# Kernel tuning notes

Measured on AMD Instinct MI355X. Metric: run time of the kernel, lower is better.

Reference implementation:

```python
import jax, jax.numpy as jnp
import numpy as np

N, E, H, L, IN, OUT = 50000, 800000, 64, 14, 128, 112
MSG_EPS = 1e-7   # GENConv message epsilon
LN_EPS = 1e-5    # torch.nn.LayerNorm default eps


def setup_inputs() -> dict:
    key = jax.random.key(0)
    ks = jax.random.split(key, 8)
    s = 0.05
    x = jax.random.normal(ks[0], (N, IN), jnp.float32)
    edge_index = jax.random.randint(ks[1], (2, E), 0, N, dtype=jnp.int64)
    enc_W = jax.random.normal(ks[2], (IN, H), jnp.float32) * s
    enc_b = jnp.zeros((H,), jnp.float32)
    ln_g = jnp.ones((L, H), jnp.float32)
    ln_b = jnp.zeros((L, H), jnp.float32)
    mlp_W = jax.random.normal(ks[3], (L, H, H), jnp.float32) * s
    mlp_b = jnp.zeros((L, H), jnp.float32)
    pred_W = jax.random.normal(ks[4], (H, OUT), jnp.float32) * s
    pred_b = jnp.zeros((OUT,), jnp.float32)
    return dict(x=x, edge_index=edge_index, enc_W=enc_W, enc_b=enc_b,
                ln_g=ln_g, ln_b=ln_b, mlp_W=mlp_W, mlp_b=mlp_b,
                pred_W=pred_W, pred_b=pred_b)


def _layernorm(h, g, b):
    mu = jnp.mean(h, axis=-1, keepdims=True)
    var = jnp.mean(jnp.square(h - mu), axis=-1, keepdims=True)  # biased, as torch
    return (h - mu) * jax.lax.rsqrt(var + LN_EPS) * g + b


def _genconv(h, src, dst, W, b):
    # GENConv: msg = relu(x_src) + eps; softmax aggregation (t=1) over dst; out = Linear(x + agg)
    msg = jax.nn.relu(h[src]) + MSG_EPS                    # [E, H]
    mmax = jax.ops.segment_max(msg, dst, num_segments=N)   # [N, H]
    mmax = jnp.where(jnp.isfinite(mmax), mmax, 0.0)         # empty segments
    ex = jnp.exp(msg - mmax[dst])                           # [E, H]
    denom = jax.ops.segment_sum(ex, dst, num_segments=N)    # [N, H]
    num = jax.ops.segment_sum(msg * ex, dst, num_segments=N)
    agg = num / jnp.maximum(denom, 1e-16)                   # 0 for isolated nodes
    return (h + agg) @ W + b


def reference(x, edge_index, enc_W, enc_b, ln_g, ln_b, mlp_W, mlp_b, pred_W, pred_b):
    src, dst = edge_index[0], edge_index[1]
    h = x @ enc_W + enc_b                       # node feature encoder
    h = _genconv(h, src, dst, mlp_W[0], mlp_b[0])  # first GCN (no pre-norm in res+)

    def body(h, params):
        g, bl, W, b = params
        h2 = jax.nn.relu(_layernorm(h, g, bl))  # dropout is identity (eval)
        h = _genconv(h2, src, dst, W, b) + h    # residual
        return h, None

    h, _ = jax.lax.scan(body, h, (ln_g[:L - 1], ln_b[:L - 1], mlp_W[1:], mlp_b[1:]))
    return h @ pred_W + pred_b
```

## Files before the change

kernel.cpp:

```cpp
#include <hip/hip_runtime.h>
#include <hip/hip_bf16.h>

#define NN 50000
#define EE 800000
#define HD 64
#define LL 14
#define IND 128
#define OUTD 112
#define LN2 0.69314718056f

typedef __attribute__((ext_vector_type(8))) short short8;
typedef __attribute__((ext_vector_type(4))) float float4_;
typedef __attribute__((ext_vector_type(4))) unsigned short ushort4_;

__device__ __forceinline__ short bf16_hi(float x) {
    return (short)(__float_as_uint(x) >> 16);
}
__device__ __forceinline__ float bf16_f(short s) {
    return __uint_as_float(((unsigned)(unsigned short)s) << 16);
}
__device__ __forceinline__ float us2f(unsigned short u) {
    return __uint_as_float(((unsigned)u) << 16);
}
__device__ __forceinline__ unsigned short f2b_rne(float x) {
    unsigned u = __float_as_uint(x);
    u += 0x7fffu + ((u >> 16) & 1u);
    return (unsigned short)(u >> 16);
}

__device__ __forceinline__ void split8(const float* p, short8& hi, short8& lo) {
    float4_ a = *(const float4_*)p;
    float4_ b = *(const float4_*)(p + 4);
    float v[8] = {a[0], a[1], a[2], a[3], b[0], b[1], b[2], b[3]};
    #pragma unroll
    for (int j = 0; j < 8; ++j) {
        short h = bf16_hi(v[j]);
        hi[j] = h;
        lo[j] = bf16_hi(v[j] - bf16_f(h));
    }
}

__device__ __forceinline__ void load_b(const float* __restrict__ W, int ldw,
                                       int colbase, int krow, short8& hi, short8& lo) {
    #pragma unroll
    for (int j = 0; j < 8; ++j) {
        float wv = W[(krow + j) * ldw + colbase];
        short h = bf16_hi(wv);
        hi[j] = h;
        lo[j] = bf16_hi(wv - bf16_f(h));
    }
}

__device__ __forceinline__ float4_ mm3(short8 ah, short8 al, short8 bh, short8 bl,
                                       float4_ acc) {
    acc = __builtin_amdgcn_mfma_f32_16x16x32_bf16(ah, bh, acc, 0, 0, 0);
    acc = __builtin_amdgcn_mfma_f32_16x16x32_bf16(al, bh, acc, 0, 0, 0);
    acc = __builtin_amdgcn_mfma_f32_16x16x32_bf16(ah, bl, acc, 0, 0, 0);
    return acc;
}


__global__ void k_hist(const int* __restrict__ ei, int* __restrict__ cnt,
                       int* __restrict__ rank) {
    int e = blockIdx.x * blockDim.x + threadIdx.x;
    if (e < EE) rank[e] = atomicAdd(&cnt[ei[EE + e]], 1);
}

__global__ __launch_bounds__(1024) void k_scan1(const int* __restrict__ deg,
                                                int* __restrict__ excl,
                                                int* __restrict__ bsum) {
    __shared__ int ws[16];
    int tid = threadIdx.x, lane = tid & 63, w = tid >> 6;
    int gid = blockIdx.x * 1024 + tid;
    int v = (gid < NN) ? deg[gid] : 0;
    int x = v;
    #pragma unroll
    for (int d = 1; d < 64; d <<= 1) {
        int y = __shfl_up(x, d);
        if (lane >= d) x += y;
    }
    if (lane == 63) ws[w] = x;
    __syncthreads();
    if (tid == 0) {
        int acc = 0;
        for (int i = 0; i < 16; i++) { int t = ws[i]; ws[i] = acc; acc += t; }
        bsum[blockIdx.x] = acc;
    }
    __syncthreads();
    if (gid < NN) excl[gid] = x - v + ws[w];
}

__global__ void k_scan2(const int* __restrict__ bsum, int* __restrict__ boff, int nb) {
    if (threadIdx.x == 0) {
        int acc = 0;
        for (int i = 0; i < nb; i++) { boff[i] = acc; acc += bsum[i]; }
    }
}

__global__ __launch_bounds__(1024) void k_scan3(int* __restrict__ rp,
                                                const int* __restrict__ boff) {
    int gid = blockIdx.x * 1024 + threadIdx.x;
    if (gid < NN) rp[gid] += boff[blockIdx.x];
    if (gid == 0) rp[NN] = EE;
}

__global__ void k_scatter(const int* __restrict__ ei, const int* __restrict__ rp,
                          const int* __restrict__ rank, int* __restrict__ csrc) {
    int e = blockIdx.x * blockDim.x + threadIdx.x;
    if (e < EE) {
        int d = ei[EE + e];
        csrc[rp[d] + rank[e]] = ei[e];
    }
}


__global__ __launch_bounds__(256) void k_enc(const float* __restrict__ x,
                                             const float* __restrict__ W,
                                             const float* __restrict__ b,
                                             float* __restrict__ h,
                                             unsigned short* __restrict__ P0) {
    __shared__ float X[16 * 132];
    int tid = threadIdx.x, lane = tid & 63, w = tid >> 6;
    int nb = blockIdx.x * 16;
    int nq = lane >> 4, nr = lane & 15;
    int colbase = w * 16 + nr;

    {
        const float* src = x + (size_t)nb * IND + tid * 8;
        float4_ a = *(const float4_*)src;
        float4_ c = *(const float4_*)(src + 4);
        int m = tid >> 4, k8 = 8 * (tid & 15);
        *(float4_*)&X[m * 132 + k8] = a;
        *(float4_*)&X[m * 132 + k8 + 4] = c;
    }
    __syncthreads();

    float4_ acc = {};
    #pragma unroll
    for (int t = 0; t < 4; ++t) {
        short8 ah, al, bh, bl;
        split8(&X[nr * 132 + t * 32 + nq * 8], ah, al);
        load_b(W, HD, colbase, t * 32 + nq * 8, bh, bl);
        acc = mm3(ah, al, bh, bl, acc);
    }

    float bias = b[colbase];
    #pragma unroll
    for (int r = 0; r < 4; ++r) {
        int node = nb + nq * 4 + r;
        float y = acc[r] + bias;
        h[node * HD + colbase] = y;
        float msg = fminf(fmaxf(y, 0.f) + 1e-7f, 50.f);
        P0[node * HD + colbase] = f2b_rne(__expf(msg));
    }
}


__global__ __launch_bounds__(256) void k_layer(const unsigned short* __restrict__ Pin,
                                               const float* __restrict__ selfh,
                                               const float* __restrict__ hres,
                                               float* __restrict__ hout,
                                               unsigned short* __restrict__ Pout,
                                               const int* __restrict__ rp,
                                               const int* __restrict__ csrc,
                                               const float* __restrict__ W,
                                               const float* __restrict__ b,
                                               const float* __restrict__ gnext,
                                               const float* __restrict__ bnext) {
    __shared__ float T[16 * 68];
    int tid = threadIdx.x, lane = tid & 63, w = tid >> 6;
    int nb = blockIdx.x * 16;
    int nq = lane >> 4, nr = lane & 15;
    int colbase = w * 16 + nr;

    short8 Bhi[2], Blo[2];
    #pragma unroll
    for (int t = 0; t < 2; ++t)
        load_b(W, HD, colbase, t * 32 + nq * 8, Bhi[t], Blo[t]);

    int g = lane >> 4;
    int ci = lane & 15;
    #pragma unroll 1
    for (int i = 0; i < 4; ++i) {
        int node = nb + w * 4 + i;
        int beg = rp[node], end = rp[node + 1], deg = end - beg;
        float s0 = 0.f, s1 = 0.f, s2 = 0.f, s3 = 0.f;
        float n0 = 0.f, n1 = 0.f, n2 = 0.f, n3 = 0.f;
        for (int chunk = 0; chunk < deg; chunk += 64) {
            int cnt = min(64, deg - chunk);
            int myidx = 0;
            if (chunk + lane < deg) myidx = csrc[beg + chunk + lane];
            int nb4 = (cnt + 3) >> 2;
            #pragma unroll 2
            for (int k = 0; k < nb4; ++k) {
                int src = __shfl(myidx, k * 4 + g);
                const unsigned* pp = (const unsigned*)(Pin + ((size_t)src << 6)) + ci * 2;
                unsigned d0 = pp[0], d1 = pp[1];
                if (k * 4 + g >= cnt) { d0 = 0u; d1 = 0u; }
                float p0 = __uint_as_float(d0 << 16);
                float p1 = __uint_as_float(d0 & 0xffff0000u);
                float p2 = __uint_as_float(d1 << 16);
                float p3 = __uint_as_float(d1 & 0xffff0000u);
                s0 += p0; s1 += p1; s2 += p2; s3 += p3;
                n0 = fmaf(p0, __log2f(fmaxf(p0, 1e-20f)), n0);
                n1 = fmaf(p1, __log2f(fmaxf(p1, 1e-20f)), n1);
                n2 = fmaf(p2, __log2f(fmaxf(p2, 1e-20f)), n2);
                n3 = fmaf(p3, __log2f(fmaxf(p3, 1e-20f)), n3);
            }
        }
        #pragma unroll
        for (int d = 16; d < 64; d <<= 1) {
            s0 += __shfl_xor(s0, d); s1 += __shfl_xor(s1, d);
            s2 += __shfl_xor(s2, d); s3 += __shfl_xor(s3, d);
            n0 += __shfl_xor(n0, d); n1 += __shfl_xor(n1, d);
            n2 += __shfl_xor(n2, d); n3 += __shfl_xor(n3, d);
        }
        if (g == 0) {
            float a0 = LN2 * n0 / fmaxf(s0, 1e-16f);
            float a1 = LN2 * n1 / fmaxf(s1, 1e-16f);
            float a2 = LN2 * n2 / fmaxf(s2, 1e-16f);
            float a3 = LN2 * n3 / fmaxf(s3, 1e-16f);
            float4_ xv;
            if (selfh) {
                float4_ sf = *(const float4_*)&selfh[(size_t)node * HD + ci * 4];
                xv[0] = sf[0] + a0; xv[1] = sf[1] + a1;
                xv[2] = sf[2] + a2; xv[3] = sf[3] + a3;
            } else {
                const unsigned* pp = (const unsigned*)(Pin + ((size_t)node << 6)) + ci * 2;
                unsigned d0 = pp[0], d1 = pp[1];
                xv[0] = LN2 * __log2f(__uint_as_float(d0 << 16)) - 1e-7f + a0;
                xv[1] = LN2 * __log2f(__uint_as_float(d0 & 0xffff0000u)) - 1e-7f + a1;
                xv[2] = LN2 * __log2f(__uint_as_float(d1 << 16)) - 1e-7f + a2;
                xv[3] = LN2 * __log2f(__uint_as_float(d1 & 0xffff0000u)) - 1e-7f + a3;
            }
            *(float4_*)&T[(w * 4 + i) * 68 + ci * 4] = xv;
        }
    }
    __syncthreads();

    short8 Ahi[2], Alo[2];
    #pragma unroll
    for (int t = 0; t < 2; ++t)
        split8(&T[nr * 68 + t * 32 + nq * 8], Ahi[t], Alo[t]);
    __syncthreads();

    float4_ acc = {};
    #pragma unroll
    for (int t = 0; t < 2; ++t)
        acc = mm3(Ahi[t], Alo[t], Bhi[t], Blo[t], acc);

    float bias = b[colbase];
    #pragma unroll
    for (int r = 0; r < 4; ++r) {
        int m = nq * 4 + r;
        int node = nb + m;
        float v = acc[r] + bias;
        if (hres) v += hres[node * HD + colbase];
        hout[node * HD + colbase] = v;
        T[m * 68 + colbase] = v;
    }
    if (!Pout) return;
    __syncthreads();

    int m = tid >> 4, c4 = (tid & 15) * 4;
    float4_ vv = *(const float4_*)&T[m * 68 + c4];
    float ps_ = (vv[0] + vv[1]) + (vv[2] + vv[3]);
    float pq_ = (vv[0] * vv[0] + vv[1] * vv[1]) + (vv[2] * vv[2] + vv[3] * vv[3]);
    #pragma unroll
    for (int d = 8; d; d >>= 1) {
        ps_ += __shfl_xor(ps_, d);
        pq_ += __shfl_xor(pq_, d);
    }
    float mu = ps_ * (1.f / 64.f);
    float var = pq_ * (1.f / 64.f) - mu * mu;
    float inv = rsqrtf(fmaxf(var, 0.f) + 1e-5f);
    float4_ g4 = *(const float4_*)&gnext[c4];
    float4_ b4 = *(const float4_*)&bnext[c4];
    ushort4_ po;
    #pragma unroll
    for (int j = 0; j < 4; ++j) {
        float y = fmaxf((vv[j] - mu) * inv * g4[j] + b4[j], 0.f);
        float msg = fminf(y + 1e-7f, 50.f);
        po[j] = f2b_rne(__expf(msg));
    }
    *(ushort4_*)&Pout[(nb + m) * HD + c4] = po;
}


__global__ __launch_bounds__(256) void k_pred(const float* __restrict__ h,
                                              const float* __restrict__ W,
                                              const float* __restrict__ b,
                                              float* __restrict__ out) {
    __shared__ float T[16 * 68];
    int tid = threadIdx.x, lane = tid & 63, w = tid >> 6;
    int nb = blockIdx.x * 16;
    int nq = lane >> 4, nr = lane & 15;

    {
        const float* src = h + (size_t)nb * HD + tid * 4;
        float4_ a = *(const float4_*)src;
        int m = tid >> 4, k4 = 4 * (tid & 15);
        *(float4_*)&T[m * 68 + k4] = a;
    }
    __syncthreads();

    short8 Ahi[2], Alo[2];
    #pragma unroll
    for (int t = 0; t < 2; ++t)
        split8(&T[nr * 68 + t * 32 + nq * 8], Ahi[t], Alo[t]);

    for (int tt = w; tt < 7; tt += 4) {
        int colbase = tt * 16 + nr;
        float4_ acc = {};
        #pragma unroll
        for (int t = 0; t < 2; ++t) {
            short8 bh, bl;
            load_b(W, OUTD, colbase, t * 32 + nq * 8, bh, bl);
            acc = mm3(Ahi[t], Alo[t], bh, bl, acc);
        }
        float bias = b[colbase];
        #pragma unroll
        for (int r = 0; r < 4; ++r) {
            int node = nb + nq * 4 + r;
            out[node * OUTD + colbase] = acc[r] + bias;
        }
    }
}


extern "C" void kernel_launch(void* const* d_in, const int* in_sizes, int n_in,
                              void* d_out, int out_size, void* d_ws, size_t ws_size,
                              hipStream_t stream) {
    const float* x    = (const float*)d_in[0];
    const int*   ei   = (const int*)d_in[1];
    const float* encW = (const float*)d_in[2];
    const float* encb = (const float*)d_in[3];
    const float* lng  = (const float*)d_in[4];
    const float* lnb  = (const float*)d_in[5];
    const float* mlpW = (const float*)d_in[6];
    const float* mlpb = (const float*)d_in[7];
    const float* pW   = (const float*)d_in[8];
    const float* pb   = (const float*)d_in[9];
    float* out = (float*)d_out;

    float* hA  = (float*)d_ws;
    float* hB  = hA + (size_t)NN * HD;
    unsigned short* PA = (unsigned short*)(hB + (size_t)NN * HD);
    unsigned short* PB = PA + (size_t)NN * HD;
    int* rp   = (int*)(PB + (size_t)NN * HD);
    int* cnt  = rp + (NN + 1);
    int* csrc = cnt + NN;
    int* rank = csrc + EE;
    int* bsum = rank + EE;
    int* boff = bsum + 64;

    hipMemsetAsync(cnt, 0, NN * sizeof(int), stream);
    k_hist<<<(EE + 255) / 256, 256, 0, stream>>>(ei, cnt, rank);
    const int NB = (NN + 1023) / 1024;
    k_scan1<<<NB, 1024, 0, stream>>>(cnt, rp, bsum);
    k_scan2<<<1, 64, 0, stream>>>(bsum, boff, NB);
    k_scan3<<<NB, 1024, 0, stream>>>(rp, boff);
    k_scatter<<<(EE + 255) / 256, 256, 0, stream>>>(ei, rp, rank, csrc);

    k_enc<<<NN / 16, 256, 0, stream>>>(x, encW, encb, hA, PA);

    k_layer<<<NN / 16, 256, 0, stream>>>(PA, hA, nullptr, hB, PB, rp, csrc,
                                         mlpW, mlpb, lng, lnb);

    float* hres = hB;
    float* hdst = hA;
    unsigned short* pc = PB;
    unsigned short* pn = PA;
    for (int l = 1; l < LL; ++l) {
        bool last = (l == LL - 1);
        k_layer<<<NN / 16, 256, 0, stream>>>(pc, nullptr, hres, hdst,
                                             last ? nullptr : pn,
                                             rp, csrc,
                                             mlpW + (size_t)l * HD * HD,
                                             mlpb + (size_t)l * HD,
                                             last ? nullptr : lng + (size_t)l * HD,
                                             last ? nullptr : lnb + (size_t)l * HD);
        float* t = hres; hres = hdst; hdst = t;
        unsigned short* u = pc; pc = pn; pn = u;
    }

    k_pred<<<NN / 16, 256, 0, stream>>>(hres, pW, pb, out);
}
```

Before: 733.9 us.

## Interleave gathers for four nodes per wave with zero sentinel row

The per-node sequential gather loop is replaced by one loop that gathers neighbours of all four nodes a wave owns at once, issuing four independent loads per iteration to raise memory-level parallelism. A zeroed sentinel row at index NN replaces per-load bounds masking, and degrees above 64 fall back to a tail loop. Launch bounds now request 4 blocks per SM. The cost is more registers and wasted loads on the sentinel row when node degrees are unbalanced.

```diff
diff --git a/kernel.cpp b/kernel.cpp
--- a/kernel.cpp
+++ b/kernel.cpp
@@ -19,9 +19,6 @@
 __device__ __forceinline__ float bf16_f(short s) {
     return __uint_as_float(((unsigned)(unsigned short)s) << 16);
 }
-__device__ __forceinline__ float us2f(unsigned short u) {
-    return __uint_as_float(((unsigned)u) << 16);
-}
 __device__ __forceinline__ unsigned short f2b_rne(float x) {
     unsigned u = __float_as_uint(x);
     u += 0x7fffu + ((u >> 16) & 1u);
@@ -58,6 +55,17 @@
     acc = __builtin_amdgcn_mfma_f32_16x16x32_bf16(ah, bl, acc, 0, 0, 0);
     return acc;
 }
+
+#define ACCQ(q, sv, nv) { \
+    float p0_ = __uint_as_float((q).x << 16); \
+    float p1_ = __uint_as_float((q).x & 0xffff0000u); \
+    float p2_ = __uint_as_float((q).y << 16); \
+    float p3_ = __uint_as_float((q).y & 0xffff0000u); \
+    sv[0] += p0_; sv[1] += p1_; sv[2] += p2_; sv[3] += p3_; \
+    nv[0] = fmaf(p0_, __log2f(fmaxf(p0_, 1e-20f)), nv[0]); \
+    nv[1] = fmaf(p1_, __log2f(fmaxf(p1_, 1e-20f)), nv[1]); \
+    nv[2] = fmaf(p2_, __log2f(fmaxf(p2_, 1e-20f)), nv[2]); \
+    nv[3] = fmaf(p3_, __log2f(fmaxf(p3_, 1e-20f)), nv[3]); }
 
 
 __global__ void k_hist(const int* __restrict__ ei, int* __restrict__ cnt,
@@ -118,12 +126,18 @@
                                              const float* __restrict__ W,
                                              const float* __restrict__ b,
                                              float* __restrict__ h,
-                                             unsigned short* __restrict__ P0) {
+                                             unsigned short* __restrict__ P0,
+                                             unsigned short* __restrict__ P1) {
     __shared__ float X[16 * 132];
     int tid = threadIdx.x, lane = tid & 63, w = tid >> 6;
     int nb = blockIdx.x * 16;
     int nq = lane >> 4, nr = lane & 15;
     int colbase = w * 16 + nr;
+
+    if (blockIdx.x == 0 && tid < HD) {
+        P0[(size_t)NN * HD + tid] = 0;
+        P1[(size_t)NN * HD + tid] = 0;
+    }
 
     {
         const float* src = x + (size_t)nb * IND + tid * 8;
@@ -155,18 +169,68 @@
     }
 }
 
-
-__global__ __launch_bounds__(256) void k_layer(const unsigned short* __restrict__ Pin,
-                                               const float* __restrict__ selfh,
-                                               const float* __restrict__ hres,
-                                               float* __restrict__ hout,
-                                               unsigned short* __restrict__ Pout,
-                                               const int* __restrict__ rp,
-                                               const int* __restrict__ csrc,
-                                               const float* __restrict__ W,
-                                               const float* __restrict__ b,
-                                               const float* __restrict__ gnext,
-                                               const float* __restrict__ bnext) {
+__device__ __forceinline__ void gtail(const unsigned* __restrict__ Pb,
+                                      const int* __restrict__ csrc,
+                                      int beg, int deg, int g, int co, int lane,
+                                      float4_& sv, float4_& nv) {
+    for (int chunk = 64; chunk < deg; chunk += 64) {
+        int my = (chunk + lane < deg) ? csrc[beg + chunk + lane] : NN;
+        int cnt = min(64, deg - chunk);
+        int nb4 = (cnt + 3) >> 2;
+        for (int k = 0; k < nb4; ++k) {
+            int e = __shfl(my, k * 4 + g);
+            uint2 q = *(const uint2*)(Pb + (((unsigned)e) << 5) + co);
+            ACCQ(q, sv, nv);
+        }
+    }
+}
+
+__device__ __forceinline__ void finish_node(float4_ sv, float4_ nv, int node, int row,
+                                            int g, int ci, int co,
+                                            const float* __restrict__ selfh,
+                                            const unsigned* __restrict__ Pb,
+                                            uint2 selfq, float* __restrict__ T) {
+    float t0 = sv[0], t1 = sv[1], t2 = sv[2], t3 = sv[3];
+    float u0 = nv[0], u1 = nv[1], u2 = nv[2], u3 = nv[3];
+    #pragma unroll
+    for (int d = 16; d < 64; d <<= 1) {
+        t0 += __shfl_xor(t0, d); t1 += __shfl_xor(t1, d);
+        t2 += __shfl_xor(t2, d); t3 += __shfl_xor(t3, d);
+        u0 += __shfl_xor(u0, d); u1 += __shfl_xor(u1, d);
+        u2 += __shfl_xor(u2, d); u3 += __shfl_xor(u3, d);
+    }
+    if (g == 0) {
+        float a0 = LN2 * u0 / fmaxf(t0, 1e-16f);
+        float a1 = LN2 * u1 / fmaxf(t1, 1e-16f);
+        float a2 = LN2 * u2 / fmaxf(t2, 1e-16f);
+        float a3 = LN2 * u3 / fmaxf(t3, 1e-16f);
+        float4_ xv;
+        if (selfh) {
+            float4_ sf = *(const float4_*)&selfh[(size_t)node * HD + ci * 4];
+            xv[0] = sf[0] + a0; xv[1] = sf[1] + a1;
+            xv[2] = sf[2] + a2; xv[3] = sf[3] + a3;
+        } else {
+            unsigned d0 = selfq.x, d1 = selfq.y;
+            xv[0] = LN2 * __log2f(__uint_as_float(d0 << 16)) - 1e-7f + a0;
+            xv[1] = LN2 * __log2f(__uint_as_float(d0 & 0xffff0000u)) - 1e-7f + a1;
+            xv[2] = LN2 * __log2f(__uint_as_float(d1 << 16)) - 1e-7f + a2;
+            xv[3] = LN2 * __log2f(__uint_as_float(d1 & 0xffff0000u)) - 1e-7f + a3;
+        }
+        *(float4_*)&T[row * 68 + ci * 4] = xv;
+    }
+}
+
+__global__ __launch_bounds__(256, 4) void k_layer(const unsigned short* __restrict__ Pin,
+                                                  const float* __restrict__ selfh,
+                                                  const float* __restrict__ hres,
+                                                  float* __restrict__ hout,
+                                                  unsigned short* __restrict__ Pout,
+                                                  const int* __restrict__ rp,
+                                                  const int* __restrict__ csrc,
+                                                  const float* __restrict__ W,
+                                                  const float* __restrict__ b,
+                                                  const float* __restrict__ gnext,
+                                                  const float* __restrict__ bnext) {
     __shared__ float T[16 * 68];
     int tid = threadIdx.x, lane = tid & 63, w = tid >> 6;
     int nb = blockIdx.x * 16;
@@ -180,62 +244,57 @@
 
     int g = lane >> 4;
     int ci = lane & 15;
-    #pragma unroll 1
-    for (int i = 0; i < 4; ++i) {
-        int node = nb + w * 4 + i;
-        int beg = rp[node], end = rp[node + 1], deg = end - beg;
-        float s0 = 0.f, s1 = 0.f, s2 = 0.f, s3 = 0.f;
-        float n0 = 0.f, n1 = 0.f, n2 = 0.f, n3 = 0.f;
-        for (int chunk = 0; chunk < deg; chunk += 64) {
-            int cnt = min(64, deg - chunk);
-            int myidx = 0;
-            if (chunk + lane < deg) myidx = csrc[beg + chunk + lane];
-            int nb4 = (cnt + 3) >> 2;
-            #pragma unroll 2
-            for (int k = 0; k < nb4; ++k) {
-                int src = __shfl(myidx, k * 4 + g);
-                const unsigned* pp = (const unsigned*)(Pin + ((size_t)src << 6)) + ci * 2;
-                unsigned d0 = pp[0], d1 = pp[1];
-                if (k * 4 + g >= cnt) { d0 = 0u; d1 = 0u; }
-                float p0 = __uint_as_float(d0 << 16);
-                float p1 = __uint_as_float(d0 & 0xffff0000u);
-                float p2 = __uint_as_float(d1 << 16);
-                float p3 = __uint_as_float(d1 & 0xffff0000u);
-                s0 += p0; s1 += p1; s2 += p2; s3 += p3;
-                n0 = fmaf(p0, __log2f(fmaxf(p0, 1e-20f)), n0);
-                n1 = fmaf(p1, __log2f(fmaxf(p1, 1e-20f)), n1);
-                n2 = fmaf(p2, __log2f(fmaxf(p2, 1e-20f)), n2);
-                n3 = fmaf(p3, __log2f(fmaxf(p3, 1e-20f)), n3);
-            }
-        }
-        #pragma unroll
-        for (int d = 16; d < 64; d <<= 1) {
-            s0 += __shfl_xor(s0, d); s1 += __shfl_xor(s1, d);
-            s2 += __shfl_xor(s2, d); s3 += __shfl_xor(s3, d);
-            n0 += __shfl_xor(n0, d); n1 += __shfl_xor(n1, d);
-            n2 += __shfl_xor(n2, d); n3 += __shfl_xor(n3, d);
-        }
-        if (g == 0) {
-            float a0 = LN2 * n0 / fmaxf(s0, 1e-16f);
-            float a1 = LN2 * n1 / fmaxf(s1, 1e-16f);
-            float a2 = LN2 * n2 / fmaxf(s2, 1e-16f);
-            float a3 = LN2 * n3 / fmaxf(s3, 1e-16f);
-            float4_ xv;
-            if (selfh) {
-                float4_ sf = *(const float4_*)&selfh[(size_t)node * HD + ci * 4];
-                xv[0] = sf[0] + a0; xv[1] = sf[1] + a1;
-                xv[2] = sf[2] + a2; xv[3] = sf[3] + a3;
-            } else {
-                const unsigned* pp = (const unsigned*)(Pin + ((size_t)node << 6)) + ci * 2;
-                unsigned d0 = pp[0], d1 = pp[1];
-                xv[0] = LN2 * __log2f(__uint_as_float(d0 << 16)) - 1e-7f + a0;
-                xv[1] = LN2 * __log2f(__uint_as_float(d0 & 0xffff0000u)) - 1e-7f + a1;
-                xv[2] = LN2 * __log2f(__uint_as_float(d1 << 16)) - 1e-7f + a2;
-                xv[3] = LN2 * __log2f(__uint_as_float(d1 & 0xffff0000u)) - 1e-7f + a3;
-            }
-            *(float4_*)&T[(w * 4 + i) * 68 + ci * 4] = xv;
-        }
-    }
+    int co = ci << 1;
+    int node0 = nb + w * 4;
+    const unsigned* Pb = (const unsigned*)Pin;
+
+    int r0 = rp[node0], r1 = rp[node0 + 1], r2 = rp[node0 + 2],
+        r3 = rp[node0 + 3], r4 = rp[node0 + 4];
+    int dA = r1 - r0, dB = r2 - r1, dC = r3 - r2, dD = r4 - r3;
+
+    int myA = (lane < dA) ? csrc[r0 + lane] : NN;
+    int myB = (lane < dB) ? csrc[r1 + lane] : NN;
+    int myC = (lane < dC) ? csrc[r2 + lane] : NN;
+    int myD = (lane < dD) ? csrc[r3 + lane] : NN;
+
+    uint2 sq0 = {0, 0}, sq1 = {0, 0}, sq2 = {0, 0}, sq3 = {0, 0};
+    if (!selfh) {
+        sq0 = *(const uint2*)(Pb + (((unsigned)(node0 + 0)) << 5) + co);
+        sq1 = *(const uint2*)(Pb + (((unsigned)(node0 + 1)) << 5) + co);
+        sq2 = *(const uint2*)(Pb + (((unsigned)(node0 + 2)) << 5) + co);
+        sq3 = *(const uint2*)(Pb + (((unsigned)(node0 + 3)) << 5) + co);
+    }
+
+    int cA = min(dA, 64), cB = min(dB, 64), cC = min(dC, 64), cD = min(dD, 64);
+    int nk = (max(max(cA, cB), max(cC, cD)) + 3) >> 2;
+
+    float4_ sA = {}, nA = {}, sB = {}, nB = {}, sC = {}, nC = {}, sD = {}, nD = {};
+
+    #pragma unroll 2
+    for (int k = 0; k < nk; ++k) {
+        int sidx = k * 4 + g;
+        int e0 = __shfl(myA, sidx);
+        int e1 = __shfl(myB, sidx);
+        int e2 = __shfl(myC, sidx);
+        int e3 = __shfl(myD, sidx);
+        uint2 q0 = *(const uint2*)(Pb + (((unsigned)e0) << 5) + co);
+        uint2 q1 = *(const uint2*)(Pb + (((unsigned)e1) << 5) + co);
+        uint2 q2 = *(const uint2*)(Pb + (((unsigned)e2) << 5) + co);
+        uint2 q3 = *(const uint2*)(Pb + (((unsigned)e3) << 5) + co);
+        ACCQ(q0, sA, nA);
+        ACCQ(q1, sB, nB);
+        ACCQ(q2, sC, nC);
+        ACCQ(q3, sD, nD);
+    }
+    if (dA > 64) gtail(Pb, csrc, r0, dA, g, co, lane, sA, nA);
+    if (dB > 64) gtail(Pb, csrc, r1, dB, g, co, lane, sB, nB);
+    if (dC > 64) gtail(Pb, csrc, r2, dC, g, co, lane, sC, nC);
+    if (dD > 64) gtail(Pb, csrc, r3, dD, g, co, lane, sD, nD);
+
+    finish_node(sA, nA, node0 + 0, w * 4 + 0, g, ci, co, selfh, Pb, sq0, T);
+    finish_node(sB, nB, node0 + 1, w * 4 + 1, g, ci, co, selfh, Pb, sq1, T);
+    finish_node(sC, nC, node0 + 2, w * 4 + 2, g, ci, co, selfh, Pb, sq2, T);
+    finish_node(sD, nD, node0 + 3, w * 4 + 3, g, ci, co, selfh, Pb, sq3, T);
     __syncthreads();
 
     short8 Ahi[2], Alo[2];
@@ -346,8 +405,8 @@
     float* hA  = (float*)d_ws;
     float* hB  = hA + (size_t)NN * HD;
     unsigned short* PA = (unsigned short*)(hB + (size_t)NN * HD);
-    unsigned short* PB = PA + (size_t)NN * HD;
-    int* rp   = (int*)(PB + (size_t)NN * HD);
+    unsigned short* PB = PA + (size_t)(NN + 1) * HD;
+    int* rp   = (int*)(PB + (size_t)(NN + 1) * HD);
     int* cnt  = rp + (NN + 1);
     int* csrc = cnt + NN;
     int* rank = csrc + EE;
@@ -362,7 +421,7 @@
     k_scan3<<<NB, 1024, 0, stream>>>(rp, boff);
     k_scatter<<<(EE + 255) / 256, 256, 0, stream>>>(ei, rp, rank, csrc);
 
-    k_enc<<<NN / 16, 256, 0, stream>>>(x, encW, encb, hA, PA);
+    k_enc<<<NN / 16, 256, 0, stream>>>(x, encW, encb, hA, PA, PB);
 
     k_layer<<<NN / 16, 256, 0, stream>>>(PA, hA, nullptr, hB, PB, rp, csrc,
                                          mlpW, mlpb, lng, lnb);
```

After: 696.7 us. 1.05x faster.

## Split fused layer kernel into separate gather and matmul kernels

Applied to the files above, without the earlier changes.

Replaces the fused per-layer kernel with a gather kernel, which gives each wave one node and each lane one feature column and unrolls the neighbor loop by four, and a separate MFMA matmul/layernorm kernel that reads the aggregated features from a new global buffer. The aim is more memory-level parallelism in the gather and simpler per-kernel scheduling. The cost is an extra global write and read of an N×64 fp32 buffer plus an extra launch per layer. The single-thread block-sum scan is also turned into a wave shuffle scan.

```diff
diff --git a/kernel.cpp b/kernel.cpp
--- a/kernel.cpp
+++ b/kernel.cpp
@@ -19,8 +19,8 @@
 __device__ __forceinline__ float bf16_f(short s) {
     return __uint_as_float(((unsigned)(unsigned short)s) << 16);
 }
-__device__ __forceinline__ float us2f(unsigned short u) {
-    return __uint_as_float(((unsigned)u) << 16);
+__device__ __forceinline__ float us2f(unsigned u) {
+    return __uint_as_float(u << 16);
 }
 __device__ __forceinline__ unsigned short f2b_rne(float x) {
     unsigned u = __float_as_uint(x);
@@ -91,10 +91,15 @@
 }
 
 __global__ void k_scan2(const int* __restrict__ bsum, int* __restrict__ boff, int nb) {
-    if (threadIdx.x == 0) {
-        int acc = 0;
-        for (int i = 0; i < nb; i++) { boff[i] = acc; acc += bsum[i]; }
-    }
+    int lane = threadIdx.x & 63;
+    int v = (lane < nb) ? bsum[lane] : 0;
+    int x = v;
+    #pragma unroll
+    for (int d = 1; d < 64; d <<= 1) {
+        int y = __shfl_up(x, d);
+        if (lane >= d) x += y;
+    }
+    if (lane < nb) boff[lane] = x - v;
 }
 
 __global__ __launch_bounds__(1024) void k_scan3(int* __restrict__ rp,
@@ -156,85 +161,72 @@
 }
 
 
-__global__ __launch_bounds__(256) void k_layer(const unsigned short* __restrict__ Pin,
-                                               const float* __restrict__ selfh,
-                                               const float* __restrict__ hres,
-                                               float* __restrict__ hout,
-                                               unsigned short* __restrict__ Pout,
-                                               const int* __restrict__ rp,
-                                               const int* __restrict__ csrc,
-                                               const float* __restrict__ W,
-                                               const float* __restrict__ b,
-                                               const float* __restrict__ gnext,
-                                               const float* __restrict__ bnext) {
+__global__ __launch_bounds__(256) void k_gather(const unsigned short* __restrict__ Pin,
+                                                const float* __restrict__ selfh,
+                                                float* __restrict__ gT,
+                                                const int* __restrict__ rp,
+                                                const int* __restrict__ csrc) {
+    int w = threadIdx.x >> 6, lane = threadIdx.x & 63;
+    int node = blockIdx.x * 4 + w;
+    int beg = rp[node], deg = rp[node + 1] - beg;
+
+    float s = 0.f, n = 0.f;
+    for (int chunk = 0; chunk < deg; chunk += 64) {
+        int cnt = min(64, deg - chunk);
+        int my = (lane < cnt) ? csrc[beg + chunk + lane] : 0;
+        int e = 0;
+        for (; e + 4 <= cnt; e += 4) {
+            int s0 = __shfl(my, e + 0);
+            int s1 = __shfl(my, e + 1);
+            int s2 = __shfl(my, e + 2);
+            int s3 = __shfl(my, e + 3);
+            float p0 = us2f(Pin[s0 * HD + lane]);
+            float p1 = us2f(Pin[s1 * HD + lane]);
+            float p2 = us2f(Pin[s2 * HD + lane]);
+            float p3 = us2f(Pin[s3 * HD + lane]);
+            n = fmaf(p0, LN2 * __log2f(p0), n); s += p0;
+            n = fmaf(p1, LN2 * __log2f(p1), n); s += p1;
+            n = fmaf(p2, LN2 * __log2f(p2), n); s += p2;
+            n = fmaf(p3, LN2 * __log2f(p3), n); s += p3;
+        }
+        for (; e < cnt; ++e) {
+            int sr = __shfl(my, e);
+            float p = us2f(Pin[sr * HD + lane]);
+            n = fmaf(p, LN2 * __log2f(p), n); s += p;
+        }
+    }
+    float agg = n / fmaxf(s, 1e-16f);
+
+    float self;
+    if (selfh) {
+        self = selfh[(size_t)node * HD + lane];
+    } else {
+        float ps = us2f(Pin[(size_t)node * HD + lane]);
+        self = LN2 * __log2f(ps) - 1e-7f;
+    }
+    gT[(size_t)node * HD + lane] = self + agg;
+}
+
+
+__global__ __launch_bounds__(256) void k_mm(const float* __restrict__ gT,
+                                            const float* __restrict__ hres,
+                                            float* __restrict__ hout,
+                                            unsigned short* __restrict__ Pout,
+                                            const float* __restrict__ W,
+                                            const float* __restrict__ b,
+                                            const float* __restrict__ gnext,
+                                            const float* __restrict__ bnext) {
     __shared__ float T[16 * 68];
     int tid = threadIdx.x, lane = tid & 63, w = tid >> 6;
     int nb = blockIdx.x * 16;
     int nq = lane >> 4, nr = lane & 15;
     int colbase = w * 16 + nr;
 
-    short8 Bhi[2], Blo[2];
-    #pragma unroll
-    for (int t = 0; t < 2; ++t)
-        load_b(W, HD, colbase, t * 32 + nq * 8, Bhi[t], Blo[t]);
-
-    int g = lane >> 4;
-    int ci = lane & 15;
-    #pragma unroll 1
-    for (int i = 0; i < 4; ++i) {
-        int node = nb + w * 4 + i;
-        int beg = rp[node], end = rp[node + 1], deg = end - beg;
-        float s0 = 0.f, s1 = 0.f, s2 = 0.f, s3 = 0.f;
-        float n0 = 0.f, n1 = 0.f, n2 = 0.f, n3 = 0.f;
-        for (int chunk = 0; chunk < deg; chunk += 64) {
-            int cnt = min(64, deg - chunk);
-            int myidx = 0;
-            if (chunk + lane < deg) myidx = csrc[beg + chunk + lane];
-            int nb4 = (cnt + 3) >> 2;
-            #pragma unroll 2
-            for (int k = 0; k < nb4; ++k) {
-                int src = __shfl(myidx, k * 4 + g);
-                const unsigned* pp = (const unsigned*)(Pin + ((size_t)src << 6)) + ci * 2;
-                unsigned d0 = pp[0], d1 = pp[1];
-                if (k * 4 + g >= cnt) { d0 = 0u; d1 = 0u; }
-                float p0 = __uint_as_float(d0 << 16);
-                float p1 = __uint_as_float(d0 & 0xffff0000u);
-                float p2 = __uint_as_float(d1 << 16);
-                float p3 = __uint_as_float(d1 & 0xffff0000u);
-                s0 += p0; s1 += p1; s2 += p2; s3 += p3;
-                n0 = fmaf(p0, __log2f(fmaxf(p0, 1e-20f)), n0);
-                n1 = fmaf(p1, __log2f(fmaxf(p1, 1e-20f)), n1);
-                n2 = fmaf(p2, __log2f(fmaxf(p2, 1e-20f)), n2);
-                n3 = fmaf(p3, __log2f(fmaxf(p3, 1e-20f)), n3);
-            }
-        }
-        #pragma unroll
-        for (int d = 16; d < 64; d <<= 1) {
-            s0 += __shfl_xor(s0, d); s1 += __shfl_xor(s1, d);
-            s2 += __shfl_xor(s2, d); s3 += __shfl_xor(s3, d);
-            n0 += __shfl_xor(n0, d); n1 += __shfl_xor(n1, d);
-            n2 += __shfl_xor(n2, d); n3 += __shfl_xor(n3, d);
-        }
-        if (g == 0) {
-            float a0 = LN2 * n0 / fmaxf(s0, 1e-16f);
-            float a1 = LN2 * n1 / fmaxf(s1, 1e-16f);
-            float a2 = LN2 * n2 / fmaxf(s2, 1e-16f);
-            float a3 = LN2 * n3 / fmaxf(s3, 1e-16f);
-            float4_ xv;
-            if (selfh) {
-                float4_ sf = *(const float4_*)&selfh[(size_t)node * HD + ci * 4];
-                xv[0] = sf[0] + a0; xv[1] = sf[1] + a1;
-                xv[2] = sf[2] + a2; xv[3] = sf[3] + a3;
-            } else {
-                const unsigned* pp = (const unsigned*)(Pin + ((size_t)node << 6)) + ci * 2;
-                unsigned d0 = pp[0], d1 = pp[1];
-                xv[0] = LN2 * __log2f(__uint_as_float(d0 << 16)) - 1e-7f + a0;
-                xv[1] = LN2 * __log2f(__uint_as_float(d0 & 0xffff0000u)) - 1e-7f + a1;
-                xv[2] = LN2 * __log2f(__uint_as_float(d1 << 16)) - 1e-7f + a2;
-                xv[3] = LN2 * __log2f(__uint_as_float(d1 & 0xffff0000u)) - 1e-7f + a3;
-            }
-            *(float4_*)&T[(w * 4 + i) * 68 + ci * 4] = xv;
-        }
+    {
+        const float* src = gT + (size_t)nb * HD + tid * 4;
+        float4_ a = *(const float4_*)src;
+        int m = tid >> 4, k4 = 4 * (tid & 15);
+        *(float4_*)&T[m * 68 + k4] = a;
     }
     __syncthreads();
 
@@ -246,8 +238,11 @@
 
     float4_ acc = {};
     #pragma unroll
-    for (int t = 0; t < 2; ++t)
-        acc = mm3(Ahi[t], Alo[t], Bhi[t], Blo[t], acc);
+    for (int t = 0; t < 2; ++t) {
+        short8 bh, bl;
+        load_b(W, HD, colbase, t * 32 + nq * 8, bh, bl);
+        acc = mm3(Ahi[t], Alo[t], bh, bl, acc);
+    }
 
     float bias = b[colbase];
     #pragma unroll
@@ -283,7 +278,7 @@
         float msg = fminf(y + 1e-7f, 50.f);
         po[j] = f2b_rne(__expf(msg));
     }
-    *(ushort4_*)&Pout[(nb + m) * HD + c4] = po;
+    *(ushort4_*)&Pout[(size_t)(nb + m) * HD + c4] = po;
 }
 
 
@@ -345,14 +340,15 @@
 
     float* hA  = (float*)d_ws;
     float* hB  = hA + (size_t)NN * HD;
-    unsigned short* PA = (unsigned short*)(hB + (size_t)NN * HD);
+    float* gT  = hB + (size_t)NN * HD;
+    unsigned short* PA = (unsigned short*)(gT + (size_t)NN * HD);
     unsigned short* PB = PA + (size_t)NN * HD;
-    int* rp   = (int*)(PB + (size_t)NN * HD);
-    int* cnt  = rp + (NN + 1);
-    int* csrc = cnt + NN;
-    int* rank = csrc + EE;
-    int* bsum = rank + EE;
-    int* boff = bsum + 64;
+    int* rp    = (int*)(PB + (size_t)NN * HD);
+    int* cnt   = rp + (NN + 1);
+    int* csrc  = cnt + NN;
+    int* rank  = csrc + EE;
+    int* bsum  = rank + EE;
+    int* boff  = bsum + 64;
 
     hipMemsetAsync(cnt, 0, NN * sizeof(int), stream);
     k_hist<<<(EE + 255) / 256, 256, 0, stream>>>(ei, cnt, rank);
@@ -364,8 +360,9 @@
 
     k_enc<<<NN / 16, 256, 0, stream>>>(x, encW, encb, hA, PA);
 
-    k_layer<<<NN / 16, 256, 0, stream>>>(PA, hA, nullptr, hB, PB, rp, csrc,
-                                         mlpW, mlpb, lng, lnb);
+    k_gather<<<NN / 4, 256, 0, stream>>>(PA, hA, gT, rp, csrc);
+    k_mm<<<NN / 16, 256, 0, stream>>>(gT, nullptr, hB, PB,
+                                      mlpW, mlpb, lng, lnb);
 
     float* hres = hB;
     float* hdst = hA;
@@ -373,13 +370,13 @@
     unsigned short* pn = PA;
     for (int l = 1; l < LL; ++l) {
         bool last = (l == LL - 1);
-        k_layer<<<NN / 16, 256, 0, stream>>>(pc, nullptr, hres, hdst,
-                                             last ? nullptr : pn,
-                                             rp, csrc,
-                                             mlpW + (size_t)l * HD * HD,
-                                             mlpb + (size_t)l * HD,
-                                             last ? nullptr : lng + (size_t)l * HD,
-                                             last ? nullptr : lnb + (size_t)l * HD);
+        k_gather<<<NN / 4, 256, 0, stream>>>(pc, nullptr, gT, rp, csrc);
+        k_mm<<<NN / 16, 256, 0, stream>>>(gT, hres, hdst,
+                                          last ? nullptr : pn,
+                                          mlpW + (size_t)l * HD * HD,
+                                          mlpb + (size_t)l * HD,
+                                          last ? nullptr : lng + (size_t)l * HD,
+                                          last ? nullptr : lnb + (size_t)l * HD);
         float* t = hres; hres = hdst; hdst = t;
         unsigned short* u = pc; pc = pn; pn = u;
     }
```

New measurement: 705.1 us. 1.04x faster.
